# Kernel tuning notes

Hardware: AMD Instinct MI355X
Metric: run time of the kernel (lower is better)

The kernel has to match this reference:

```python
import jax, jax.numpy as jnp
import numpy as np

N = 100000
E = 1600000
HID = 64
FLAT = 4
PI = np.pi


def _mlp(x, W1, b1, W2, b2, W3, b3):
    h = jax.nn.silu(x @ W1 + b1)
    h = jax.nn.silu(h @ W2 + b2)
    return h @ W3 + b3


def _forward(h_i_real, h_i_imag, edge_index, node_params, edge_params,
             Wa, ba, Wr1, br1, Wr2, br2, Wr3, br3, Wi1, bi1, Wi2, bi2, Wi3, bi3):
    sender = edge_index[0]
    receiver = edge_index[1]
    En = sender.shape[0]
    hr_s = h_i_real[sender].reshape(En, -1)
    hr_r = h_i_real[receiver].reshape(En, -1)
    hi_s = h_i_imag[sender].reshape(En, -1)
    hi_r = h_i_imag[receiver].reshape(En, -1)
    # faithful to torch: edge_params[edge_index] is [2,E,1], then row-major view(E,2)
    ep = edge_params[edge_index].reshape(En, -1)
    np_s = node_params[sender]
    np_r = node_params[receiver]
    A_real = _mlp(jnp.concatenate([hr_s, hr_r, np_s, np_r, ep], axis=1), Wr1, br1, Wr2, br2, Wr3, br3)
    A_imag = _mlp(jnp.concatenate([hi_s, hi_r, np_s, np_r, ep], axis=1), Wi1, bi1, Wi2, bi2, Wi3, bi3)
    angles = jnp.tanh(jnp.concatenate([A_imag, A_real], axis=1) @ Wa + ba)
    m_ij = angles * PI  # [E,3] Euler angle messages
    n_nodes = node_params.shape[0]
    agg = jax.ops.segment_sum(m_ij, receiver, num_segments=n_nodes)
    agg = (agg + PI) % (2.0 * PI) - PI  # wrap to (-pi, pi]
    a = agg[:, 0]
    b = agg[:, 1]
    c = agg[:, 2]
    cb = jnp.cos(0.5 * b)
    sb = jnp.sin(0.5 * b)
    # closed-form U = exp(-i a sz/2) exp(-i b sy/2) exp(-i c sz/2)  (ZYZ Euler rotation)
    e_mm = jnp.exp(-0.5j * (a + c))
    e_pp = jnp.exp(0.5j * (a + c))
    e_md = jnp.exp(-0.5j * (a - c))
    e_pd = jnp.exp(0.5j * (a - c))
    row0 = jnp.stack([e_mm * cb, -(e_md * sb)], axis=-1)
    row1 = jnp.stack([e_pd * sb, e_pp * cb], axis=-1)
    U = jnp.stack([row0, row1], axis=-2)  # [N,2,2] complex64, unitary by construction
    Ud = jnp.conj(jnp.swapaxes(U, -1, -2))
    h = (h_i_real + 1j * h_i_imag).astype(jnp.complex64)
    return jnp.matmul(U, jnp.matmul(h, Ud))


def setup_inputs():
    key = jax.random.key(0)
    ks = jax.random.split(key, 16)

    def rn(k, shape, scale=1.0):
        return (jax.random.normal(k, shape, jnp.float32) * scale).astype(jnp.float32)

    IN = 2 * FLAT + 2 * 2 + 2 * 1  # 14
    inp = {
        "h_i_real": rn(ks[0], (N, 2, 2)),
        "h_i_imag": rn(ks[1], (N, 2, 2)),
        "edge_index": jax.random.randint(ks[2], (2, E), 0, N, dtype=jnp.int32),
        "node_params": rn(ks[3], (N, 2)),
        "edge_params": rn(ks[4], (N, 1)),
        "Wa": rn(ks[5], (2 * FLAT, 3), 1.0 / np.sqrt(2 * FLAT)),
        "ba": jnp.zeros((3,), jnp.float32),
    }
    s1 = 1.0 / np.sqrt(IN)
    s2 = 1.0 / np.sqrt(HID)
    for pfx, k0 in (("r", 6), ("i", 9)):
        inp["W%s1" % pfx] = rn(ks[k0], (IN, HID), s1)
        inp["b%s1" % pfx] = jnp.zeros((HID,), jnp.float32)
        inp["W%s2" % pfx] = rn(ks[k0 + 1], (HID, HID), s2)
        inp["b%s2" % pfx] = jnp.zeros((HID,), jnp.float32)
        inp["W%s3" % pfx] = rn(ks[k0 + 2], (HID, FLAT), s2)
        inp["b%s3" % pfx] = jnp.zeros((FLAT,), jnp.float32)
    return inp


def reference(h_i_real, h_i_imag, edge_index, node_params, edge_params,
              Wa, ba, Wr1, br1, Wr2, br2, Wr3, br3, Wi1, bi1, Wi2, bi2, Wi3, bi3):
    return _forward(h_i_real, h_i_imag, edge_index, node_params, edge_params,
                    Wa, ba, Wr1, br1, Wr2, br2, Wr3, br3, Wi1, bi1, Wi2, bi2, Wi3, bi3)
```

## Files before the change

kernel.cpp:

```cpp
#include <hip/hip_runtime.h>

#define PI_F     3.14159265358979323846f
#define TWO_PI_F 6.28318530717958647692f

typedef __attribute__((ext_vector_type(8))) _Float16 half8;
typedef __attribute__((ext_vector_type(4))) float f32x4;

#define LO_SCALE   2048.0f
#define LO_INV     (1.0f / 2048.0f)

__device__ __forceinline__ float fast_rcp(float x) { return __builtin_amdgcn_rcpf(x); }
__device__ __forceinline__ float silu_f(float v) { return v * fast_rcp(1.0f + __expf(-v)); }
__device__ __forceinline__ float tanh_f(float z) {
    float ez = __expf(2.0f * z);
    return 1.0f - 2.0f * fast_rcp(ez + 1.0f);
}

#define WS_U16_TOTAL 28672
#define WS_BYTES_NEEDED (WS_U16_TOTAL * 2)
#define W_HI_U16 14336

__global__ __launch_bounds__(256) void qgnn_prep_kernel(
    const float* __restrict__ Wr1, const float* __restrict__ Wr2, const float* __restrict__ Wr3,
    const float* __restrict__ Wi1, const float* __restrict__ Wi2, const float* __restrict__ Wi3,
    unsigned short* __restrict__ wsu)
{
    int idx = blockIdx.x * 256 + threadIdx.x;
    if (idx >= 14336) return;
    int rel = idx;
    int half = (rel >= 7168);
    if (half) rel -= 7168;
    const float* W; int base, NT, Kr, Nr;
    if (rel < 2048)      { W = half ? Wi1 : Wr1; base = 0;    NT = 4; Kr = 14; Nr = 64; }
    else if (rel < 6144) { W = half ? Wi2 : Wr2; base = 2048; NT = 4; Kr = 64; Nr = 64; }
    else                 { W = half ? Wi3 : Wr3; base = 6144; NT = 1; Kr = 64; Nr = 4;  }
    int f = rel - base;
    int frag = f >> 9, rem = f & 511;
    int l = rem >> 3, j = rem & 7;
    int nt = frag % NT, kt = frag / NT;
    int k = kt * 32 + ((l >> 4) << 3) + j;
    int n = nt * 16 + (l & 15);
    float v = (k < Kr && n < Nr) ? W[k * Nr + n] : 0.0f;
    _Float16 hi = (_Float16)v;
    _Float16 lo = (_Float16)((v - (float)hi) * LO_SCALE);
    wsu[idx] = *reinterpret_cast<unsigned short*>(&hi);
    wsu[14336 + idx] = *reinterpret_cast<unsigned short*>(&lo);
}

__global__ __launch_bounds__(256) void qgnn_zero_kernel(float* __restrict__ p, int n) {
    const int i = blockIdx.x * blockDim.x + threadIdx.x;
    if (i < n) p[i] = 0.0f;
}

#define MFMA16(a, b, c) __builtin_amdgcn_mfma_f32_16x16x32_f16((a), (b), (c), 0, 0, 0)
#define NW 4

__device__ __forceinline__ void run_mlp(
    half8 ah, half8 als,
    const _Float16* __restrict__ wh,
    const unsigned short* __restrict__ wls,
    f32x4 b1v, f32x4 b2v, float b3v,
    _Float16* __restrict__ H, float* __restrict__ h3out,
    int lane, int m16, int g)
{
    #pragma unroll 2
    for (int nt = 0; nt < 4; ++nt) {
        const float bv = b1v[nt];
        f32x4 accm = {bv, bv, bv, bv};
        f32x4 accc = {0.f, 0.f, 0.f, 0.f};
        const half8 bh  = *reinterpret_cast<const half8*>(&wh[(nt * 64 + lane) * 8]);
        const half8 bls = *reinterpret_cast<const half8*>(&wls[(nt * 64 + lane) * 8]);
        accm = MFMA16(ah, bh, accm);
        accc = MFMA16(als, bh, accc);
        accc = MFMA16(ah, bls, accc);
        #pragma unroll
        for (int i = 0; i < 4; ++i) {
            const float hv = silu_f(accm[i] + accc[i] * LO_INV);
            H[(4 * g + i) * 72 + nt * 16 + m16] = (_Float16)hv;
        }
    }

    {
        const half8 a0 = *reinterpret_cast<const half8*>(&H[m16 * 72 + 8 * g]);
        const half8 a1 = *reinterpret_cast<const half8*>(&H[m16 * 72 + 32 + 8 * g]);
        #pragma unroll 2
        for (int nt = 0; nt < 4; ++nt) {
            const float bv = b2v[nt];
            f32x4 accm = {bv, bv, bv, bv};
            f32x4 accc = {0.f, 0.f, 0.f, 0.f};
            const half8 bh0  = *reinterpret_cast<const half8*>(&wh[2048 + ((0 * 4 + nt) * 64 + lane) * 8]);
            const half8 bls0 = *reinterpret_cast<const half8*>(&wls[2048 + ((0 * 4 + nt) * 64 + lane) * 8]);
            const half8 bh1  = *reinterpret_cast<const half8*>(&wh[2048 + ((1 * 4 + nt) * 64 + lane) * 8]);
            const half8 bls1 = *reinterpret_cast<const half8*>(&wls[2048 + ((1 * 4 + nt) * 64 + lane) * 8]);
            accm = MFMA16(a0, bh0, accm);
            accm = MFMA16(a1, bh1, accm);
            accc = MFMA16(a0, bls0, accc);
            accc = MFMA16(a1, bls1, accc);
            #pragma unroll
            for (int i = 0; i < 4; ++i) {
                const float hv = silu_f(accm[i] + accc[i] * LO_INV);
                H[(4 * g + i) * 72 + nt * 16 + m16] = (_Float16)hv;
            }
        }
    }

    {
        const half8 a0 = *reinterpret_cast<const half8*>(&H[m16 * 72 + 8 * g]);
        const half8 a1 = *reinterpret_cast<const half8*>(&H[m16 * 72 + 32 + 8 * g]);
        f32x4 accm = {b3v, b3v, b3v, b3v};
        f32x4 accc = {0.f, 0.f, 0.f, 0.f};
        const half8 bh0  = *reinterpret_cast<const half8*>(&wh[6144 + (0 * 64 + lane) * 8]);
        const half8 bls0 = *reinterpret_cast<const half8*>(&wls[6144 + (0 * 64 + lane) * 8]);
        const half8 bh1  = *reinterpret_cast<const half8*>(&wh[6144 + (1 * 64 + lane) * 8]);
        const half8 bls1 = *reinterpret_cast<const half8*>(&wls[6144 + (1 * 64 + lane) * 8]);
        accm = MFMA16(a0, bh0, accm);
        accm = MFMA16(a1, bh1, accm);
        accc = MFMA16(a0, bls0, accc);
        accc = MFMA16(a1, bls1, accc);
        if (m16 < 4) {
            #pragma unroll
            for (int i = 0; i < 4; ++i)
                h3out[(4 * g + i) * 8 + m16] = accm[i] + accc[i] * LO_INV;
        }
    }
}

__global__ __launch_bounds__(256, 3) void qgnn_edge_mfma_kernel(
    const float* __restrict__ hr, const float* __restrict__ hi_,
    const int* __restrict__ ei,
    const float* __restrict__ npar, const float* __restrict__ epar,
    const float* __restrict__ Wa, const float* __restrict__ ba,
    const float* __restrict__ br1, const float* __restrict__ br2, const float* __restrict__ br3,
    const float* __restrict__ bi1, const float* __restrict__ bi2, const float* __restrict__ bi3,
    const unsigned short* __restrict__ wsu,
    float* __restrict__ aggout, int E, int stride)
{
    __shared__ __align__(16) _Float16 sW[W_HI_U16];
    __shared__ __align__(16) _Float16 sH[NW][16 * 72];
    __shared__ __align__(16) float sH3[NW][16 * 8];

    {
        unsigned short* sWu = reinterpret_cast<unsigned short*>(sW);
        for (int o = threadIdx.x * 8; o < W_HI_U16; o += 256 * 8)
            *reinterpret_cast<uint4*>(sWu + o) = *reinterpret_cast<const uint4*>(wsu + o);
    }
    __syncthreads();

    const int tid = threadIdx.x, w = tid >> 6, lane = tid & 63;
    const int m16 = lane & 15, g = lane >> 4;
    _Float16* H = sH[w];
    float* H3 = sH3[w];

    f32x4 br1v, br2v, bi1v, bi2v;
    #pragma unroll
    for (int q = 0; q < 4; ++q) {
        br1v[q] = br1[q * 16 + m16];
        br2v[q] = br2[q * 16 + m16];
        bi1v[q] = bi1[q * 16 + m16];
        bi2v[q] = bi2[q * 16 + m16];
    }
    const float br3v = (m16 < 4) ? br3[m16] : 0.0f;
    const float bi3v = (m16 < 4) ? bi3[m16] : 0.0f;
    float wav[24], bav[3];
    #pragma unroll
    for (int q = 0; q < 24; ++q) wav[q] = Wa[q];
    #pragma unroll
    for (int q = 0; q < 3; ++q) bav[q] = ba[q];

    const int ntiles = (E + 15) >> 4;
    for (int tile = blockIdx.x * NW + w; tile < ntiles; tile += gridDim.x * NW) {
        const int em = tile * 16 + m16;
        const bool valid = (em < E);

        float f0[8], f1[8];
        #pragma unroll
        for (int j = 0; j < 8; ++j) { f0[j] = 0.0f; f1[j] = 0.0f; }
        if (valid && g < 2) {
            const int s = ei[em], r = ei[E + em];
            if (g == 0) {
                const float4 a = *reinterpret_cast<const float4*>(hr  + 4 * (size_t)s);
                const float4 b = *reinterpret_cast<const float4*>(hr  + 4 * (size_t)r);
                const float4 c = *reinterpret_cast<const float4*>(hi_ + 4 * (size_t)s);
                const float4 d = *reinterpret_cast<const float4*>(hi_ + 4 * (size_t)r);
                f0[0] = a.x; f0[1] = a.y; f0[2] = a.z; f0[3] = a.w;
                f0[4] = b.x; f0[5] = b.y; f0[6] = b.z; f0[7] = b.w;
                f1[0] = c.x; f1[1] = c.y; f1[2] = c.z; f1[3] = c.w;
                f1[4] = d.x; f1[5] = d.y; f1[6] = d.z; f1[7] = d.w;
            } else {
                const float2 n0 = *reinterpret_cast<const float2*>(npar + 2 * (size_t)s);
                const float2 n1 = *reinterpret_cast<const float2*>(npar + 2 * (size_t)r);
                const float e0 = epar[ei[2 * em + 0]];
                const float e1 = epar[ei[2 * em + 1]];
                f0[0] = n0.x; f0[1] = n0.y; f0[2] = n1.x; f0[3] = n1.y;
                f0[4] = e0;   f0[5] = e1;
                #pragma unroll
                for (int j = 0; j < 6; ++j) f1[j] = f0[j];
            }
        }
        half8 xh0, xls0, xh1, xls1;
        #pragma unroll
        for (int j = 0; j < 8; ++j) {
            const _Float16 h0 = (_Float16)f0[j];
            xh0[j] = h0;
            xls0[j] = (_Float16)((f0[j] - (float)h0) * LO_SCALE);
            const _Float16 h1 = (_Float16)f1[j];
            xh1[j] = h1;
            xls1[j] = (_Float16)((f1[j] - (float)h1) * LO_SCALE);
        }

        run_mlp(xh0, xls0, sW, wsu + W_HI_U16,
                br1v, br2v, br3v, H, H3 + 0, lane, m16, g);
        run_mlp(xh1, xls1, sW + 7168, wsu + W_HI_U16 + 7168,
                bi1v, bi2v, bi3v, H, H3 + 4, lane, m16, g);

        if (lane < 16) {
            const int e2 = tile * 16 + lane;
            if (e2 < E) {
                const float4 Ai4 = *reinterpret_cast<const float4*>(&H3[lane * 8 + 4]);
                const float4 Ar4 = *reinterpret_cast<const float4*>(&H3[lane * 8 + 0]);
                const float Ai[4] = {Ai4.x, Ai4.y, Ai4.z, Ai4.w};
                const float Ar[4] = {Ar4.x, Ar4.y, Ar4.z, Ar4.w};
                const int r = ei[E + e2];
                #pragma unroll
                for (int t = 0; t < 3; ++t) {
                    float z = bav[t];
                    #pragma unroll
                    for (int j = 0; j < 4; ++j) z += Ai[j] * wav[j * 3 + t];
                    #pragma unroll
                    for (int j = 0; j < 4; ++j) z += Ar[j] * wav[(4 + j) * 3 + t];
                    atomicAdd(aggout + (size_t)stride * (size_t)r + t, tanh_f(z) * PI_F);
                }
            }
        }
    }
}

__device__ __forceinline__ void mlp14_64_64_4(
    const float x[14],
    const float* __restrict__ W1, const float* __restrict__ b1,
    const float* __restrict__ W2, const float* __restrict__ b2,
    const float* __restrict__ W3, const float* __restrict__ b3,
    float A[4])
{
    float h1[64];
    #pragma unroll
    for (int j = 0; j < 64; ++j) h1[j] = b1[j];
    #pragma unroll
    for (int k = 0; k < 14; ++k) {
        const float xk = x[k];
        #pragma unroll
        for (int j = 0; j < 64; ++j) h1[j] += xk * W1[k * 64 + j];
    }
    #pragma unroll
    for (int j = 0; j < 64; ++j) h1[j] = silu_f(h1[j]);
    float h2[64];
    #pragma unroll
    for (int j = 0; j < 64; ++j) h2[j] = b2[j];
    #pragma unroll
    for (int k = 0; k < 64; ++k) {
        const float hk = h1[k];
        #pragma unroll
        for (int j = 0; j < 64; ++j) h2[j] += hk * W2[k * 64 + j];
    }
    #pragma unroll
    for (int j = 0; j < 64; ++j) h2[j] = silu_f(h2[j]);
    float a0 = b3[0], a1 = b3[1], a2 = b3[2], a3 = b3[3];
    #pragma unroll
    for (int k = 0; k < 64; ++k) {
        const float hk = h2[k];
        a0 += hk * W3[k * 4 + 0];
        a1 += hk * W3[k * 4 + 1];
        a2 += hk * W3[k * 4 + 2];
        a3 += hk * W3[k * 4 + 3];
    }
    A[0] = a0; A[1] = a1; A[2] = a2; A[3] = a3;
}

template<int STRIDE>
__global__ __launch_bounds__(256) void qgnn_edge_kernel(
    const float* __restrict__ hr, const float* __restrict__ hi,
    const int* __restrict__ ei,
    const float* __restrict__ npar, const float* __restrict__ epar,
    const float* __restrict__ Wa, const float* __restrict__ ba,
    const float* __restrict__ Wr1, const float* __restrict__ br1,
    const float* __restrict__ Wr2, const float* __restrict__ br2,
    const float* __restrict__ Wr3, const float* __restrict__ br3,
    const float* __restrict__ Wi1, const float* __restrict__ bi1,
    const float* __restrict__ Wi2, const float* __restrict__ bi2,
    const float* __restrict__ Wi3, const float* __restrict__ bi3,
    float* __restrict__ aggout, int E)
{
    const int e = blockIdx.x * blockDim.x + threadIdx.x;
    if (e >= E) return;
    const int s = ei[e];
    const int r = ei[E + e];
    const float ep0 = epar[ei[2 * e + 0]];
    const float ep1 = epar[ei[2 * e + 1]];
    const float4 hrs = *reinterpret_cast<const float4*>(hr + 4 * (size_t)s);
    const float4 hrr = *reinterpret_cast<const float4*>(hr + 4 * (size_t)r);
    const float2 nps = *reinterpret_cast<const float2*>(npar + 2 * (size_t)s);
    const float2 npr = *reinterpret_cast<const float2*>(npar + 2 * (size_t)r);
    float x[14];
    x[0] = hrs.x; x[1] = hrs.y; x[2] = hrs.z; x[3] = hrs.w;
    x[4] = hrr.x; x[5] = hrr.y; x[6] = hrr.z; x[7] = hrr.w;
    x[8] = nps.x; x[9] = nps.y; x[10] = npr.x; x[11] = npr.y;
    x[12] = ep0;  x[13] = ep1;
    float Ar[4];
    mlp14_64_64_4(x, Wr1, br1, Wr2, br2, Wr3, br3, Ar);
    const float4 his = *reinterpret_cast<const float4*>(hi + 4 * (size_t)s);
    const float4 hir = *reinterpret_cast<const float4*>(hi + 4 * (size_t)r);
    x[0] = his.x; x[1] = his.y; x[2] = his.z; x[3] = his.w;
    x[4] = hir.x; x[5] = hir.y; x[6] = hir.z; x[7] = hir.w;
    float Ai[4];
    mlp14_64_64_4(x, Wi1, bi1, Wi2, bi2, Wi3, bi3, Ai);
    #pragma unroll
    for (int t = 0; t < 3; ++t) {
        float z = ba[t];
        #pragma unroll
        for (int j = 0; j < 4; ++j) z += Ai[j] * Wa[j * 3 + t];
        #pragma unroll
        for (int j = 0; j < 4; ++j) z += Ar[j] * Wa[(4 + j) * 3 + t];
        atomicAdd(aggout + (size_t)STRIDE * (size_t)r + t, tanh_f(z) * PI_F);
    }
}

__device__ __forceinline__ float wrap_pi(float v) {
    float rm = fmodf(v + PI_F, TWO_PI_F);
    if (rm < 0.0f) rm += TWO_PI_F;
    return rm - PI_F;
}

template<int STRIDE, bool WRITE_COMPLEX>
__global__ __launch_bounds__(256) void qgnn_node_kernel(
    const float* __restrict__ hr,
    const float* __restrict__ hi,
    float* __restrict__ out, int N)
{
    const int n = blockIdx.x * blockDim.x + threadIdx.x;
    if (n >= N) return;
    const float a = wrap_pi(out[(size_t)STRIDE * n + 0]);
    const float b = wrap_pi(out[(size_t)STRIDE * n + 1]);
    const float c = wrap_pi(out[(size_t)STRIDE * n + 2]);
    const float cb = __cosf(0.5f * b);
    const float sb = __sinf(0.5f * b);
    const float hpc = 0.5f * (a + c);
    const float hmc = 0.5f * (a - c);
    const float cpc = __cosf(hpc), spc = __sinf(hpc);
    const float cmc = __cosf(hmc), smc = __sinf(hmc);
    float Ur[2][2], Ui[2][2];
    Ur[0][0] =  cpc * cb;  Ui[0][0] = -spc * cb;
    Ur[0][1] = -cmc * sb;  Ui[0][1] =  smc * sb;
    Ur[1][0] =  cmc * sb;  Ui[1][0] =  smc * sb;
    Ur[1][1] =  cpc * cb;  Ui[1][1] =  spc * cb;
    const float4 h4r = *reinterpret_cast<const float4*>(hr + 4 * (size_t)n);
    const float4 h4i = *reinterpret_cast<const float4*>(hi + 4 * (size_t)n);
    float Hr[2][2] = {{h4r.x, h4r.y}, {h4r.z, h4r.w}};
    float Hi[2][2] = {{h4i.x, h4i.y}, {h4i.z, h4i.w}};
    float Tr[2][2], Ti[2][2];
    #pragma unroll
    for (int p = 0; p < 2; ++p) {
        #pragma unroll
        for (int j = 0; j < 2; ++j) {
            float tr = 0.0f, ti = 0.0f;
            #pragma unroll
            for (int t = 0; t < 2; ++t) {
                tr += Hr[p][t] * Ur[j][t] + Hi[p][t] * Ui[j][t];
                ti += Hi[p][t] * Ur[j][t] - Hr[p][t] * Ui[j][t];
            }
            Tr[p][j] = tr; Ti[p][j] = ti;
        }
    }
    float orr[2][2], oii[2][2];
    #pragma unroll
    for (int i = 0; i < 2; ++i) {
        #pragma unroll
        for (int j = 0; j < 2; ++j) {
            float xr = 0.0f, xi = 0.0f;
            #pragma unroll
            for (int p = 0; p < 2; ++p) {
                xr += Ur[i][p] * Tr[p][j] - Ui[i][p] * Ti[p][j];
                xi += Ur[i][p] * Ti[p][j] + Ui[i][p] * Tr[p][j];
            }
            orr[i][j] = xr; oii[i][j] = xi;
        }
    }
    if (WRITE_COMPLEX) {
        float4* outv = reinterpret_cast<float4*>(out + (size_t)STRIDE * n);
        outv[0] = make_float4(orr[0][0], oii[0][0], orr[0][1], oii[0][1]);
        outv[1] = make_float4(orr[1][0], oii[1][0], orr[1][1], oii[1][1]);
    } else {
        *reinterpret_cast<float4*>(out + (size_t)STRIDE * n) =
            make_float4(orr[0][0], orr[0][1], orr[1][0], orr[1][1]);
    }
}

extern "C" void kernel_launch(void* const* d_in, const int* in_sizes, int n_in,
                              void* d_out, int out_size, void* d_ws, size_t ws_size,
                              hipStream_t stream) {
    const float* hr   = (const float*)d_in[0];
    const float* hi   = (const float*)d_in[1];
    const int*   ei   = (const int*)  d_in[2];
    const float* npar = (const float*)d_in[3];
    const float* epar = (const float*)d_in[4];
    const float* Wa  = (const float*)d_in[5];
    const float* ba  = (const float*)d_in[6];
    const float* Wr1 = (const float*)d_in[7];
    const float* br1 = (const float*)d_in[8];
    const float* Wr2 = (const float*)d_in[9];
    const float* br2 = (const float*)d_in[10];
    const float* Wr3 = (const float*)d_in[11];
    const float* br3 = (const float*)d_in[12];
    const float* Wi1 = (const float*)d_in[13];
    const float* bi1 = (const float*)d_in[14];
    const float* Wi2 = (const float*)d_in[15];
    const float* bi2 = (const float*)d_in[16];
    const float* Wi3 = (const float*)d_in[17];
    const float* bi3 = (const float*)d_in[18];

    const int N = in_sizes[0] / 4;
    const int E = in_sizes[2] / 2;

    float* out = (float*)d_out;
    const bool cplx = (out_size >= 8 * N);
    const int stride = cplx ? 8 : 4;
    const int total = stride * N;
    qgnn_zero_kernel<<<(total + 255) / 256, 256, 0, stream>>>(out, total);

    const bool use_mfma = (ws_size >= (size_t)WS_BYTES_NEEDED);
    if (use_mfma) {
        qgnn_prep_kernel<<<56, 256, 0, stream>>>(Wr1, Wr2, Wr3, Wi1, Wi2, Wi3,
                                                 (unsigned short*)d_ws);
        const int ntiles = (E + 15) / 16;
        int blocks = (ntiles + NW - 1) / NW;
        if (blocks > 4096) blocks = 4096;
        qgnn_edge_mfma_kernel<<<blocks, 256, 0, stream>>>(
            hr, hi, ei, npar, epar, Wa, ba,
            br1, br2, br3, bi1, bi2, bi3,
            (const unsigned short*)d_ws, out, E, stride);
    } else if (cplx) {
        qgnn_edge_kernel<8><<<(E + 255) / 256, 256, 0, stream>>>(
            hr, hi, ei, npar, epar, Wa, ba,
            Wr1, br1, Wr2, br2, Wr3, br3,
            Wi1, bi1, Wi2, bi2, Wi3, bi3, out, E);
    } else {
        qgnn_edge_kernel<4><<<(E + 255) / 256, 256, 0, stream>>>(
            hr, hi, ei, npar, epar, Wa, ba,
            Wr1, br1, Wr2, br2, Wr3, br3,
            Wi1, bi1, Wi2, bi2, Wi3, bi3, out, E);
    }

    if (cplx) {
        qgnn_node_kernel<8, true><<<(N + 255) / 256, 256, 0, stream>>>(hr, hi, out, N);
    } else {
        qgnn_node_kernel<4, false><<<(N + 255) / 256, 256, 0, stream>>>(hr, hi, out, N);
    }
}
```

Baseline: 292.6 us.

## Process two 16-edge subtiles per wave and fold layer-1 bias into weights

Each wave now handles 32 edges per iteration as two 16-row MFMA subtiles that share every loaded weight fragment (high part from LDS, low-correction part from global). This halves the weight-fragment loads per edge and gives more independent MFMAs to interleave. The layer-1 bias is folded into the weight matrix as an extra input row fed by a constant 1.0 feature. In exchange, register and LDS use per wave roughly double, which may lower occupancy under the 3-blocks-per-SM launch bound.

```diff
diff --git a/kernel.cpp b/kernel.cpp
--- a/kernel.cpp
+++ b/kernel.cpp
@@ -8,6 +8,7 @@
 
 #define LO_SCALE   2048.0f
 #define LO_INV     (1.0f / 2048.0f)
+#define RS 72
 
 __device__ __forceinline__ float fast_rcp(float x) { return __builtin_amdgcn_rcpf(x); }
 __device__ __forceinline__ float silu_f(float v) { return v * fast_rcp(1.0f + __expf(-v)); }
@@ -23,6 +24,7 @@
 __global__ __launch_bounds__(256) void qgnn_prep_kernel(
     const float* __restrict__ Wr1, const float* __restrict__ Wr2, const float* __restrict__ Wr3,
     const float* __restrict__ Wi1, const float* __restrict__ Wi2, const float* __restrict__ Wi3,
+    const float* __restrict__ br1, const float* __restrict__ bi1,
     unsigned short* __restrict__ wsu)
 {
     int idx = blockIdx.x * 256 + threadIdx.x;
@@ -30,8 +32,8 @@
     int rel = idx;
     int half = (rel >= 7168);
     if (half) rel -= 7168;
-    const float* W; int base, NT, Kr, Nr;
-    if (rel < 2048)      { W = half ? Wi1 : Wr1; base = 0;    NT = 4; Kr = 14; Nr = 64; }
+    const float* W; int base, NT, Kr, Nr; bool isL1 = false;
+    if (rel < 2048)      { W = half ? Wi1 : Wr1; base = 0;    NT = 4; Kr = 14; Nr = 64; isL1 = true; }
     else if (rel < 6144) { W = half ? Wi2 : Wr2; base = 2048; NT = 4; Kr = 64; Nr = 64; }
     else                 { W = half ? Wi3 : Wr3; base = 6144; NT = 1; Kr = 64; Nr = 4;  }
     int f = rel - base;
@@ -40,7 +42,9 @@
     int nt = frag % NT, kt = frag / NT;
     int k = kt * 32 + ((l >> 4) << 3) + j;
     int n = nt * 16 + (l & 15);
-    float v = (k < Kr && n < Nr) ? W[k * Nr + n] : 0.0f;
+    float v = 0.0f;
+    if (k < Kr && n < Nr) v = W[k * Nr + n];
+    else if (isL1 && k == 14) v = (half ? bi1 : br1)[n];
     _Float16 hi = (_Float16)v;
     _Float16 lo = (_Float16)((v - (float)hi) * LO_SCALE);
     wsu[idx] = *reinterpret_cast<unsigned short*>(&hi);
@@ -55,72 +59,86 @@
 #define MFMA16(a, b, c) __builtin_amdgcn_mfma_f32_16x16x32_f16((a), (b), (c), 0, 0, 0)
 #define NW 4
 
-__device__ __forceinline__ void run_mlp(
-    half8 ah, half8 als,
+__device__ __forceinline__ void run_mlp2(
+    half8 ahA, half8 alsA, half8 ahB, half8 alsB,
     const _Float16* __restrict__ wh,
     const unsigned short* __restrict__ wls,
-    f32x4 b1v, f32x4 b2v, float b3v,
+    f32x4 b2v, float b3v,
     _Float16* __restrict__ H, float* __restrict__ h3out,
     int lane, int m16, int g)
 {
+    const f32x4 ZERO4 = {0.f, 0.f, 0.f, 0.f};
+
     #pragma unroll 2
     for (int nt = 0; nt < 4; ++nt) {
-        const float bv = b1v[nt];
-        f32x4 accm = {bv, bv, bv, bv};
-        f32x4 accc = {0.f, 0.f, 0.f, 0.f};
-        const half8 bh  = *reinterpret_cast<const half8*>(&wh[(nt * 64 + lane) * 8]);
-        const half8 bls = *reinterpret_cast<const half8*>(&wls[(nt * 64 + lane) * 8]);
-        accm = MFMA16(ah, bh, accm);
-        accc = MFMA16(als, bh, accc);
-        accc = MFMA16(ah, bls, accc);
+        const half8 bh = *reinterpret_cast<const half8*>(&wh[(nt * 64 + lane) * 8]);
+        const half8 bl = *reinterpret_cast<const half8*>(&wls[(nt * 64 + lane) * 8]);
+        f32x4 amA = MFMA16(ahA, bh, ZERO4);
+        f32x4 acA = MFMA16(alsA, bh, ZERO4);
+        acA = MFMA16(ahA, bl, acA);
+        f32x4 amB = MFMA16(ahB, bh, ZERO4);
+        f32x4 acB = MFMA16(alsB, bh, ZERO4);
+        acB = MFMA16(ahB, bl, acB);
         #pragma unroll
         for (int i = 0; i < 4; ++i) {
-            const float hv = silu_f(accm[i] + accc[i] * LO_INV);
-            H[(4 * g + i) * 72 + nt * 16 + m16] = (_Float16)hv;
+            const int col = nt * 16 + m16;
+            H[(4 * g + i) * RS + col]        = (_Float16)silu_f(amA[i] + acA[i] * LO_INV);
+            H[(16 + 4 * g + i) * RS + col]   = (_Float16)silu_f(amB[i] + acB[i] * LO_INV);
         }
     }
 
     {
-        const half8 a0 = *reinterpret_cast<const half8*>(&H[m16 * 72 + 8 * g]);
-        const half8 a1 = *reinterpret_cast<const half8*>(&H[m16 * 72 + 32 + 8 * g]);
-        #pragma unroll 2
+        const half8 a0A = *reinterpret_cast<const half8*>(&H[m16 * RS + 8 * g]);
+        const half8 a1A = *reinterpret_cast<const half8*>(&H[m16 * RS + 32 + 8 * g]);
+        const half8 a0B = *reinterpret_cast<const half8*>(&H[(16 + m16) * RS + 8 * g]);
+        const half8 a1B = *reinterpret_cast<const half8*>(&H[(16 + m16) * RS + 32 + 8 * g]);
+        #pragma unroll 1
         for (int nt = 0; nt < 4; ++nt) {
+            const half8 bh0 = *reinterpret_cast<const half8*>(&wh[2048 + ((0 * 4 + nt) * 64 + lane) * 8]);
+            const half8 bl0 = *reinterpret_cast<const half8*>(&wls[2048 + ((0 * 4 + nt) * 64 + lane) * 8]);
+            const half8 bh1 = *reinterpret_cast<const half8*>(&wh[2048 + ((1 * 4 + nt) * 64 + lane) * 8]);
+            const half8 bl1 = *reinterpret_cast<const half8*>(&wls[2048 + ((1 * 4 + nt) * 64 + lane) * 8]);
+            f32x4 amA = MFMA16(a0A, bh0, ZERO4);
+            amA = MFMA16(a1A, bh1, amA);
+            f32x4 acA = MFMA16(a0A, bl0, ZERO4);
+            acA = MFMA16(a1A, bl1, acA);
+            f32x4 amB = MFMA16(a0B, bh0, ZERO4);
+            amB = MFMA16(a1B, bh1, amB);
+            f32x4 acB = MFMA16(a0B, bl0, ZERO4);
+            acB = MFMA16(a1B, bl1, acB);
             const float bv = b2v[nt];
-            f32x4 accm = {bv, bv, bv, bv};
-            f32x4 accc = {0.f, 0.f, 0.f, 0.f};
-            const half8 bh0  = *reinterpret_cast<const half8*>(&wh[2048 + ((0 * 4 + nt) * 64 + lane) * 8]);
-            const half8 bls0 = *reinterpret_cast<const half8*>(&wls[2048 + ((0 * 4 + nt) * 64 + lane) * 8]);
-            const half8 bh1  = *reinterpret_cast<const half8*>(&wh[2048 + ((1 * 4 + nt) * 64 + lane) * 8]);
-            const half8 bls1 = *reinterpret_cast<const half8*>(&wls[2048 + ((1 * 4 + nt) * 64 + lane) * 8]);
-            accm = MFMA16(a0, bh0, accm);
-            accm = MFMA16(a1, bh1, accm);
-            accc = MFMA16(a0, bls0, accc);
-            accc = MFMA16(a1, bls1, accc);
             #pragma unroll
             for (int i = 0; i < 4; ++i) {
-                const float hv = silu_f(accm[i] + accc[i] * LO_INV);
-                H[(4 * g + i) * 72 + nt * 16 + m16] = (_Float16)hv;
+                const int col = nt * 16 + m16;
+                H[(4 * g + i) * RS + col]      = (_Float16)silu_f(amA[i] + acA[i] * LO_INV + bv);
+                H[(16 + 4 * g + i) * RS + col] = (_Float16)silu_f(amB[i] + acB[i] * LO_INV + bv);
             }
         }
     }
 
     {
-        const half8 a0 = *reinterpret_cast<const half8*>(&H[m16 * 72 + 8 * g]);
-        const half8 a1 = *reinterpret_cast<const half8*>(&H[m16 * 72 + 32 + 8 * g]);
-        f32x4 accm = {b3v, b3v, b3v, b3v};
-        f32x4 accc = {0.f, 0.f, 0.f, 0.f};
-        const half8 bh0  = *reinterpret_cast<const half8*>(&wh[6144 + (0 * 64 + lane) * 8]);
-        const half8 bls0 = *reinterpret_cast<const half8*>(&wls[6144 + (0 * 64 + lane) * 8]);
-        const half8 bh1  = *reinterpret_cast<const half8*>(&wh[6144 + (1 * 64 + lane) * 8]);
-        const half8 bls1 = *reinterpret_cast<const half8*>(&wls[6144 + (1 * 64 + lane) * 8]);
-        accm = MFMA16(a0, bh0, accm);
-        accm = MFMA16(a1, bh1, accm);
-        accc = MFMA16(a0, bls0, accc);
-        accc = MFMA16(a1, bls1, accc);
+        const half8 a0A = *reinterpret_cast<const half8*>(&H[m16 * RS + 8 * g]);
+        const half8 a1A = *reinterpret_cast<const half8*>(&H[m16 * RS + 32 + 8 * g]);
+        const half8 a0B = *reinterpret_cast<const half8*>(&H[(16 + m16) * RS + 8 * g]);
+        const half8 a1B = *reinterpret_cast<const half8*>(&H[(16 + m16) * RS + 32 + 8 * g]);
+        const half8 bh0 = *reinterpret_cast<const half8*>(&wh[6144 + (0 * 64 + lane) * 8]);
+        const half8 bl0 = *reinterpret_cast<const half8*>(&wls[6144 + (0 * 64 + lane) * 8]);
+        const half8 bh1 = *reinterpret_cast<const half8*>(&wh[6144 + (1 * 64 + lane) * 8]);
+        const half8 bl1 = *reinterpret_cast<const half8*>(&wls[6144 + (1 * 64 + lane) * 8]);
+        f32x4 amA = MFMA16(a0A, bh0, ZERO4);
+        amA = MFMA16(a1A, bh1, amA);
+        f32x4 acA = MFMA16(a0A, bl0, ZERO4);
+        acA = MFMA16(a1A, bl1, acA);
+        f32x4 amB = MFMA16(a0B, bh0, ZERO4);
+        amB = MFMA16(a1B, bh1, amB);
+        f32x4 acB = MFMA16(a0B, bl0, ZERO4);
+        acB = MFMA16(a1B, bl1, acB);
         if (m16 < 4) {
             #pragma unroll
-            for (int i = 0; i < 4; ++i)
-                h3out[(4 * g + i) * 8 + m16] = accm[i] + accc[i] * LO_INV;
+            for (int i = 0; i < 4; ++i) {
+                h3out[(4 * g + i) * 8 + m16]        = amA[i] + acA[i] * LO_INV + b3v;
+                h3out[(16 + 4 * g + i) * 8 + m16]   = amB[i] + acB[i] * LO_INV + b3v;
+            }
         }
     }
 }
@@ -130,14 +148,14 @@
     const int* __restrict__ ei,
     const float* __restrict__ npar, const float* __restrict__ epar,
     const float* __restrict__ Wa, const float* __restrict__ ba,
-    const float* __restrict__ br1, const float* __restrict__ br2, const float* __restrict__ br3,
-    const float* __restrict__ bi1, const float* __restrict__ bi2, const float* __restrict__ bi3,
+    const float* __restrict__ br2, const float* __restrict__ br3,
+    const float* __restrict__ bi2, const float* __restrict__ bi3,
     const unsigned short* __restrict__ wsu,
     float* __restrict__ aggout, int E, int stride)
 {
     __shared__ __align__(16) _Float16 sW[W_HI_U16];
-    __shared__ __align__(16) _Float16 sH[NW][16 * 72];
-    __shared__ __align__(16) float sH3[NW][16 * 8];
+    __shared__ __align__(16) _Float16 sH[NW][32 * RS];
+    __shared__ __align__(16) float sH3[NW][32 * 8];
 
     {
         unsigned short* sWu = reinterpret_cast<unsigned short*>(sW);
@@ -151,12 +169,10 @@
     _Float16* H = sH[w];
     float* H3 = sH3[w];
 
-    f32x4 br1v, br2v, bi1v, bi2v;
+    f32x4 br2v, bi2v;
     #pragma unroll
     for (int q = 0; q < 4; ++q) {
-        br1v[q] = br1[q * 16 + m16];
         br2v[q] = br2[q * 16 + m16];
-        bi1v[q] = bi1[q * 16 + m16];
         bi2v[q] = bi2[q * 16 + m16];
     }
     const float br3v = (m16 < 4) ? br3[m16] : 0.0f;
@@ -167,59 +183,67 @@
     #pragma unroll
     for (int q = 0; q < 3; ++q) bav[q] = ba[q];
 
-    const int ntiles = (E + 15) >> 4;
+    const _Float16*       whR = sW;
+    const _Float16*       whI = sW + 7168;
+    const unsigned short* wlR = wsu + W_HI_U16;
+    const unsigned short* wlI = wsu + W_HI_U16 + 7168;
+
+    const int ntiles = (E + 31) >> 5;
     for (int tile = blockIdx.x * NW + w; tile < ntiles; tile += gridDim.x * NW) {
-        const int em = tile * 16 + m16;
-        const bool valid = (em < E);
-
-        float f0[8], f1[8];
-        #pragma unroll
-        for (int j = 0; j < 8; ++j) { f0[j] = 0.0f; f1[j] = 0.0f; }
-        if (valid && g < 2) {
-            const int s = ei[em], r = ei[E + em];
-            if (g == 0) {
-                const float4 a = *reinterpret_cast<const float4*>(hr  + 4 * (size_t)s);
-                const float4 b = *reinterpret_cast<const float4*>(hr  + 4 * (size_t)r);
-                const float4 c = *reinterpret_cast<const float4*>(hi_ + 4 * (size_t)s);
-                const float4 d = *reinterpret_cast<const float4*>(hi_ + 4 * (size_t)r);
-                f0[0] = a.x; f0[1] = a.y; f0[2] = a.z; f0[3] = a.w;
-                f0[4] = b.x; f0[5] = b.y; f0[6] = b.z; f0[7] = b.w;
-                f1[0] = c.x; f1[1] = c.y; f1[2] = c.z; f1[3] = c.w;
-                f1[4] = d.x; f1[5] = d.y; f1[6] = d.z; f1[7] = d.w;
-            } else {
-                const float2 n0 = *reinterpret_cast<const float2*>(npar + 2 * (size_t)s);
-                const float2 n1 = *reinterpret_cast<const float2*>(npar + 2 * (size_t)r);
-                const float e0 = epar[ei[2 * em + 0]];
-                const float e1 = epar[ei[2 * em + 1]];
-                f0[0] = n0.x; f0[1] = n0.y; f0[2] = n1.x; f0[3] = n1.y;
-                f0[4] = e0;   f0[5] = e1;
-                #pragma unroll
-                for (int j = 0; j < 6; ++j) f1[j] = f0[j];
-            }
-        }
-        half8 xh0, xls0, xh1, xls1;
-        #pragma unroll
-        for (int j = 0; j < 8; ++j) {
-            const _Float16 h0 = (_Float16)f0[j];
-            xh0[j] = h0;
-            xls0[j] = (_Float16)((f0[j] - (float)h0) * LO_SCALE);
-            const _Float16 h1 = (_Float16)f1[j];
-            xh1[j] = h1;
-            xls1[j] = (_Float16)((f1[j] - (float)h1) * LO_SCALE);
-        }
-
-        run_mlp(xh0, xls0, sW, wsu + W_HI_U16,
-                br1v, br2v, br3v, H, H3 + 0, lane, m16, g);
-        run_mlp(xh1, xls1, sW + 7168, wsu + W_HI_U16 + 7168,
-                bi1v, bi2v, bi3v, H, H3 + 4, lane, m16, g);
-
-        if (lane < 16) {
-            const int e2 = tile * 16 + lane;
+        half8 xh0A, xls0A, xh1A, xls1A, xh0B, xls0B, xh1B, xls1B;
+        #pragma unroll
+        for (int hb = 0; hb < 2; ++hb) {
+            const int em = tile * 32 + hb * 16 + m16;
+            const bool valid = (em < E);
+            float f0[8], f1[8];
+            #pragma unroll
+            for (int j = 0; j < 8; ++j) { f0[j] = 0.0f; f1[j] = 0.0f; }
+            if (valid && g < 2) {
+                const int s = ei[em], r = ei[E + em];
+                if (g == 0) {
+                    const float4 a = *reinterpret_cast<const float4*>(hr  + 4 * (size_t)s);
+                    const float4 b = *reinterpret_cast<const float4*>(hr  + 4 * (size_t)r);
+                    const float4 c = *reinterpret_cast<const float4*>(hi_ + 4 * (size_t)s);
+                    const float4 d = *reinterpret_cast<const float4*>(hi_ + 4 * (size_t)r);
+                    f0[0] = a.x; f0[1] = a.y; f0[2] = a.z; f0[3] = a.w;
+                    f0[4] = b.x; f0[5] = b.y; f0[6] = b.z; f0[7] = b.w;
+                    f1[0] = c.x; f1[1] = c.y; f1[2] = c.z; f1[3] = c.w;
+                    f1[4] = d.x; f1[5] = d.y; f1[6] = d.z; f1[7] = d.w;
+                } else {
+                    const float2 n0 = *reinterpret_cast<const float2*>(npar + 2 * (size_t)s);
+                    const float2 n1 = *reinterpret_cast<const float2*>(npar + 2 * (size_t)r);
+                    const float e0 = epar[ei[2 * em + 0]];
+                    const float e1 = epar[ei[2 * em + 1]];
+                    f0[0] = n0.x; f0[1] = n0.y; f0[2] = n1.x; f0[3] = n1.y;
+                    f0[4] = e0;   f0[5] = e1;   f0[6] = 1.0f;
+                    #pragma unroll
+                    for (int j = 0; j < 7; ++j) f1[j] = f0[j];
+                }
+            }
+            half8 xh0, xls0, xh1, xls1;
+            #pragma unroll
+            for (int j = 0; j < 8; ++j) {
+                const _Float16 h0 = (_Float16)f0[j];
+                xh0[j] = h0;
+                xls0[j] = (_Float16)((f0[j] - (float)h0) * LO_SCALE);
+                const _Float16 h1 = (_Float16)f1[j];
+                xh1[j] = h1;
+                xls1[j] = (_Float16)((f1[j] - (float)h1) * LO_SCALE);
+            }
+            if (hb == 0) { xh0A = xh0; xls0A = xls0; xh1A = xh1; xls1A = xls1; }
+            else         { xh0B = xh0; xls0B = xls0; xh1B = xh1; xls1B = xls1; }
+        }
+
+        run_mlp2(xh0A, xls0A, xh0B, xls0B, whR, wlR, br2v, br3v, H, H3 + 0, lane, m16, g);
+        run_mlp2(xh1A, xls1A, xh1B, xls1B, whI, wlI, bi2v, bi3v, H, H3 + 4, lane, m16, g);
+
+        if (lane < 32) {
+            const int e2 = tile * 32 + lane;
             if (e2 < E) {
+                const float4 Ar4 = *reinterpret_cast<const float4*>(&H3[lane * 8 + 0]);
                 const float4 Ai4 = *reinterpret_cast<const float4*>(&H3[lane * 8 + 4]);
-                const float4 Ar4 = *reinterpret_cast<const float4*>(&H3[lane * 8 + 0]);
+                const float Ar[4] = {Ar4.x, Ar4.y, Ar4.z, Ar4.w};
                 const float Ai[4] = {Ai4.x, Ai4.y, Ai4.z, Ai4.w};
-                const float Ar[4] = {Ar4.x, Ar4.y, Ar4.z, Ar4.w};
                 const int r = ei[E + e2];
                 #pragma unroll
                 for (int t = 0; t < 3; ++t) {
@@ -429,13 +453,13 @@
     const bool use_mfma = (ws_size >= (size_t)WS_BYTES_NEEDED);
     if (use_mfma) {
         qgnn_prep_kernel<<<56, 256, 0, stream>>>(Wr1, Wr2, Wr3, Wi1, Wi2, Wi3,
-                                                 (unsigned short*)d_ws);
-        const int ntiles = (E + 15) / 16;
+                                                 br1, bi1, (unsigned short*)d_ws);
+        const int ntiles = (E + 31) / 32;
         int blocks = (ntiles + NW - 1) / NW;
         if (blocks > 4096) blocks = 4096;
         qgnn_edge_mfma_kernel<<<blocks, 256, 0, stream>>>(
             hr, hi, ei, npar, epar, Wa, ba,
-            br1, br2, br3, bi1, bi2, bi3,
+            br2, br3, bi2, bi3,
             (const unsigned short*)d_ws, out, E, stride);
     } else if (cplx) {
         qgnn_edge_kernel<8><<<(E + 255) / 256, 256, 0, stream>>>(
```

Result: no change. 296.6 us (+1.4%).
